# Performance work log

Measured on AMD Instinct MI355X. Metric: run time of the kernel, lower is better.

## Reference

```python
import jax, jax.numpy as jnp
import numpy as np
import math


def _layernorm(x, g, b, eps=1e-5):
    m = x.mean(-1, keepdims=True)
    v = x.var(-1, keepdims=True)
    return (x - m) / jnp.sqrt(v + eps) * g + b


def _ssd(log_decay, frequency, b_r, b_i, chunk):
    # SSD eigenstate evolution: chunk-local complex decay-mask matmuls + sequential inter-chunk state scan
    B, T, K = b_r.shape
    T_pad = -(-T // chunk) * chunk
    if T_pad > T:
        pad = T_pad - T
        b_r = jnp.pad(b_r, ((0, 0), (0, pad), (0, 0)))
        b_i = jnp.pad(b_i, ((0, 0), (0, pad), (0, 0)))
    n_chunks = T_pad // chunk
    mag = jax.nn.sigmoid(log_decay)                      # (K,)
    pos = jnp.arange(chunk, dtype=b_r.dtype)             # (C,)
    mag_pow = mag[None, :] ** pos[:, None]               # (C,K)
    phases = pos[:, None] * frequency[None, :]           # (C,K)
    kernel_r = mag_pow * jnp.cos(phases)
    kernel_i = mag_pow * jnp.sin(phases)
    diffs = pos[None, :] - pos[:, None]                  # (C,C), faithful to torch: pos.unsqueeze(0)-pos.unsqueeze(1)
    mask = (diffs >= 0).astype(b_r.dtype)[:, :, None]
    idx = jnp.clip(diffs, 0, None).astype(jnp.int32)
    L_r = kernel_r[idx] * mask                           # (C,C,K)
    L_i = kernel_i[idx] * mask
    Br = b_r.reshape(B, n_chunks, chunk, K)
    Bi = b_i.reshape(B, n_chunks, chunk, K)
    # intra-chunk complex contraction
    intra_r = jnp.einsum('ijk,bnjk->bnik', L_r, Br) - jnp.einsum('ijk,bnjk->bnik', L_i, Bi)
    intra_i = jnp.einsum('ijk,bnjk->bnik', L_r, Bi) + jnp.einsum('ijk,bnjk->bnik', L_i, Br)
    prop_r = L_r[:, 0, :]                                # (C,K)
    prop_i = L_i[:, 0, :]

    def step(carry, chunk_in):
        sr, si = carry                                   # (B,K)
        ir, ii = chunk_in                                # (B,C,K)
        corr_r = prop_r[None] * sr[:, None] - prop_i[None] * si[:, None]
        corr_i = prop_r[None] * si[:, None] + prop_i[None] * sr[:, None]
        out_r = ir + corr_r
        out_i = ii + corr_i
        return (out_r[:, -1], out_i[:, -1]), (out_r, out_i)

    init = (jnp.zeros((B, K), b_r.dtype), jnp.zeros((B, K), b_r.dtype))
    _, (o_r, o_i) = jax.lax.scan(step, init, (intra_r.transpose(1, 0, 2, 3), intra_i.transpose(1, 0, 2, 3)))
    c_r = o_r.transpose(1, 0, 2, 3).reshape(B, T_pad, K)[:, :T]
    c_i = o_i.transpose(1, 0, 2, 3).reshape(B, T_pad, K)[:, :T]
    return c_r, c_i


def setup_inputs() -> dict:
    B, T, D, K, H, CONV = 4, 4096, 1024, 64, 4, 4
    Kh = K // H
    mlp = 4 * D
    ks = jax.random.split(jax.random.key(0), 12)

    def n(k, shape, s):
        return (jax.random.normal(k, shape) * s).astype(jnp.float32)

    return {
        'x': n(ks[0], (B, T, D), 1.0),
        'in_proj_w': n(ks[1], (2 * K, D), 1.0 / math.sqrt(D)),
        'conv_w': n(ks[2], (2 * K, 1, CONV), 0.5),
        'conv_b': jnp.zeros((2 * K,), jnp.float32),
        'log_decay': jax.random.uniform(ks[3], (K,), minval=-3.0, maxval=-1.5).astype(jnp.float32),
        'frequency': jnp.linspace(0.0, 2 * math.pi * (1 - 1.0 / K), K).astype(jnp.float32),
        'coupling': (jnp.eye(Kh)[None] + 0.01 * jax.random.normal(ks[4], (H, Kh, Kh)) / math.sqrt(Kh)).astype(jnp.float32),
        'out_proj_w': n(ks[5], (D, 2 * K), 1.0 / math.sqrt(2 * K)),
        'gate_w': n(ks[6], (D, D), 1.0 / math.sqrt(D)),
        'gate_b': jnp.full((D,), -2.0, jnp.float32),
        'mlp_w1': n(ks[7], (mlp, D), 1.0 / math.sqrt(D)),
        'mlp_b1': jnp.zeros((mlp,), jnp.float32),
        'mlp_w2': n(ks[8], (D, mlp), 1.0 / math.sqrt(mlp)),
        'mlp_b2': jnp.zeros((D,), jnp.float32),
        'ln1_g': jnp.ones((D,), jnp.float32), 'ln1_b': jnp.zeros((D,), jnp.float32),
        'ln2_g': jnp.ones((D,), jnp.float32), 'ln2_b': jnp.zeros((D,), jnp.float32),
    }


def reference(x, in_proj_w, conv_w, conv_b, log_decay, frequency, coupling,
              out_proj_w, gate_w, gate_b, mlp_w1, mlp_b1, mlp_w2, mlp_b2,
              ln1_g, ln1_b, ln2_g, ln2_b):
    B, T, D = x.shape
    K2 = in_proj_w.shape[0]
    K = K2 // 2
    CHUNK = 64
    H, Kh = coupling.shape[0], coupling.shape[1]
    residual = x
    xn = _layernorm(x, ln1_g, ln1_b)
    beta = xn @ in_proj_w.T                              # (B,T,2K)
    kconv = conv_w.shape[-1]
    # causal depthwise conv1d (torch pads both sides then truncates to T == left-pad kconv-1)
    bc = jax.lax.conv_general_dilated(
        beta.transpose(0, 2, 1), conv_w, (1,), [(kconv - 1, 0)],
        feature_group_count=K2, dimension_numbers=('NCH', 'OIH', 'NCH'))
    beta = jax.nn.silu((bc + conv_b[None, :, None]).transpose(0, 2, 1))
    beta_r, beta_i = beta[..., :K], beta[..., K:]
    c_r, c_i = _ssd(log_decay, frequency, beta_r, beta_i, CHUNK)
    c_r = jnp.einsum('hjk,bthk->bthj', coupling, c_r.reshape(B, T, H, Kh)).reshape(B, T, K)
    c_i = jnp.einsum('hjk,bthk->bthj', coupling, c_i.reshape(B, T, H, Kh)).reshape(B, T, K)
    eig = jnp.concatenate([c_r, c_i], axis=-1)           # (B,T,2K)
    h = eig @ out_proj_w.T
    gate = jax.nn.sigmoid(xn @ gate_w.T + gate_b)
    x1 = residual + gate * h
    xn2 = _layernorm(x1, ln2_g, ln2_b)
    out = x1 + (jax.nn.silu(xn2 @ mlp_w1.T + mlp_b1) @ mlp_w2.T + mlp_b2)
    return out, eig
```

## Files before the change

kernel.cpp:

```cpp
#include <hip/hip_runtime.h>
#include <hip/hip_bf16.h>


#define FIR_LAG 20

typedef __attribute__((ext_vector_type(8))) short    bf16x8;
typedef __attribute__((ext_vector_type(4))) float    f32x4;
typedef __attribute__((ext_vector_type(4))) unsigned short ushort4_t;

__device__ __forceinline__ unsigned short f2bf(float f) {
    union { __hip_bfloat16 b; unsigned short u; } cv;
    cv.b = __float2bfloat16(f);
    return cv.u;
}
__device__ __forceinline__ float bf2f(unsigned short u) {
    return __uint_as_float((unsigned)u << 16);
}

__device__ __forceinline__ void gload_lds16(const unsigned short* g, unsigned short* l) {
    __builtin_amdgcn_global_load_lds(
        (const __attribute__((address_space(1))) unsigned int*)g,
        (__attribute__((address_space(3))) unsigned int*)l, 16, 0, 0);
}

__global__ __launch_bounds__(256) void cvt_bf16_kernel(
    const float* __restrict__ in, unsigned short* __restrict__ out, int n)
{
    int i = (blockIdx.x * 256 + threadIdx.x) * 8;
    if (i >= n) return;
    float4 a = *(const float4*)(in + i);
    float4 b = *(const float4*)(in + i + 4);
    ushort4_t o0 = { f2bf(a.x), f2bf(a.y), f2bf(a.z), f2bf(a.w) };
    ushort4_t o1 = { f2bf(b.x), f2bf(b.y), f2bf(b.z), f2bf(b.w) };
    *(ushort4_t*)(out + i)     = o0;
    *(ushort4_t*)(out + i + 4) = o1;
}

__global__ __launch_bounds__(256) void ln_kernel(
    const float* __restrict__ in, const float* __restrict__ g,
    const float* __restrict__ b, unsigned short* __restrict__ out)
{
    const size_t row = blockIdx.x;
    const int t = threadIdx.x;
    float4 v = ((const float4*)(in + row * 1024))[t];
    float s  = v.x + v.y + v.z + v.w;
    float s2 = v.x*v.x + v.y*v.y + v.z*v.z + v.w*v.w;
    #pragma unroll
    for (int o = 32; o > 0; o >>= 1) {
        s  += __shfl_down(s, o);
        s2 += __shfl_down(s2, o);
    }
    __shared__ float red[8];
    __shared__ float mv[2];
    const int wv = t >> 6;
    if ((t & 63) == 0) { red[wv] = s; red[4 + wv] = s2; }
    __syncthreads();
    if (t == 0) {
        float a  = red[0] + red[1] + red[2] + red[3];
        float a2 = red[4] + red[5] + red[6] + red[7];
        float mean = a * (1.f / 1024.f);
        float var  = a2 * (1.f / 1024.f) - mean * mean;
        mv[0] = mean;
        mv[1] = rsqrtf(var + 1e-5f);
    }
    __syncthreads();
    const float mean = mv[0], rstd = mv[1];
    float4 gg = ((const float4*)g)[t];
    float4 bb = ((const float4*)b)[t];
    ushort4_t o4 = { f2bf((v.x - mean) * rstd * gg.x + bb.x),
                     f2bf((v.y - mean) * rstd * gg.y + bb.y),
                     f2bf((v.z - mean) * rstd * gg.z + bb.z),
                     f2bf((v.w - mean) * rstd * gg.w + bb.w) };
    *(ushort4_t*)(out + row * 1024 + t * 4) = o4;
}

__global__ __launch_bounds__(256) void conv_silu_kernel(
    const float* __restrict__ bp, const float* __restrict__ cw,
    const float* __restrict__ cb, float* __restrict__ beta, int T)
{
    const int idx = blockIdx.x * 256 + threadIdx.x;
    const int c  = idx & 127;
    const int bt = idx >> 7;
    const int t  = bt & (T - 1);
    float acc = cb[c];
    #pragma unroll
    for (int j = 0; j < 4; ++j) {
        int ts = t - 3 + j;
        if (ts >= 0) acc += cw[c * 4 + j] * bp[(size_t)(bt - 3 + j) * 128 + c];
    }
    beta[(size_t)bt * 128 + c] = acc / (1.f + expf(-acc));
}

__global__ __launch_bounds__(256) void fir_coupling_kernel(
    const float* __restrict__ beta, const float* __restrict__ log_decay,
    const float* __restrict__ freq, const float* __restrict__ coup,
    float* __restrict__ eig, unsigned short* __restrict__ eig_bf, int T)
{
    __shared__ float sb[65][128];
    const int blk = blockIdx.x;
    const int nch = T >> 6;
    const int b = blk / nch;
    const int n = blk - b * nch;
    const size_t base = ((size_t)b * T + (size_t)n * 64) * 128;
    const int tid = threadIdx.x;

    #pragma unroll
    for (int it = 0; it < 8; ++it) {
        int f = tid + it * 256;
        int r = f >> 5, c4 = f & 31;
        *(float4*)&sb[1 + r][c4 * 4] =
            *(const float4*)(beta + base + (size_t)r * 128 + c4 * 4);
    }
    if (tid < 32) {
        float4 z = make_float4(0.f, 0.f, 0.f, 0.f);
        *(float4*)&sb[0][tid * 4] =
            (n > 0) ? *(const float4*)(beta + base - 128 + tid * 4) : z;
    }
    __syncthreads();

    const int k  = tid & 63;
    const int tq = tid >> 6;
    const float mag = 1.f / (1.f + expf(-log_decay[k]));
    const float w = freq[k];
    const float rr = mag * cosf(w), ri = mag * sinf(w);
    float cr[16], ci[16];
    #pragma unroll
    for (int m = 0; m < 16; ++m) { cr[m] = 0.f; ci[m] = 0.f; }
    float zr = 1.f, zi = 0.f;
    for (int e = 0; e <= FIR_LAG; ++e) {
        #pragma unroll
        for (int m = 0; m < 16; ++m) {
            int i = tq * 16 + m;
            int src = i + e;
            if (src <= 63) {
                float br = sb[1 + src][k];
                float bi = sb[1 + src][64 + k];
                cr[m] += zr * br - zi * bi;
                ci[m] += zr * bi + zi * br;
            }
        }
        float nzr = zr * rr - zi * ri;
        zi = zr * ri + zi * rr;
        zr = nzr;
    }
    if (tq == 0) {
        cr[0] += sb[0][k];
        ci[0] += sb[0][64 + k];
    }
    __syncthreads();
    #pragma unroll
    for (int m = 0; m < 16; ++m) {
        int i = tq * 16 + m;
        sb[i][k] = cr[m];
        sb[i][64 + k] = ci[m];
    }
    __syncthreads();
    const int h = k >> 4, j = k & 15;
    float cp[16];
    #pragma unroll
    for (int q = 0; q < 16; ++q) cp[q] = coup[(h * 16 + j) * 16 + q];
    #pragma unroll
    for (int m = 0; m < 16; ++m) {
        int i = tq * 16 + m;
        float sr = 0.f, si = 0.f;
        #pragma unroll
        for (int q = 0; q < 16; ++q) {
            sr += cp[q] * sb[i][h * 16 + q];
            si += cp[q] * sb[i][64 + h * 16 + q];
        }
        size_t o = base + (size_t)i * 128;
        eig[o + k]         = sr;
        eig[o + 64 + k]    = si;
        eig_bf[o + k]      = f2bf(sr);
        eig_bf[o + 64 + k] = f2bf(si);
    }
}

__global__ __launch_bounds__(256) void gemm_mfma_f32out(
    const unsigned short* __restrict__ A, const unsigned short* __restrict__ B,
    float* __restrict__ C, int M, int N, int K)
{
    constexpr int BM = 128, BK = 32;
    __shared__ unsigned short As[BM * BK];
    __shared__ unsigned short Bs[BM * BK];
    const int tid  = threadIdx.x;
    const int lane = tid & 63;
    const int wave = tid >> 6;
    const int wm = wave >> 1, wn = wave & 1;
    const int bm = blockIdx.y * BM;
    const int bn = blockIdx.x * BM;

    f32x4 acc[4][4];
    #pragma unroll
    for (int m = 0; m < 4; ++m)
        #pragma unroll
        for (int n = 0; n < 4; ++n) acc[m][n] = (f32x4){0.f, 0.f, 0.f, 0.f};

    const int frow = lane & 15;
    const int fk   = (lane >> 4) * 8;
    const int srow = tid >> 2;
    const int sc   = (tid & 3) * 8;

    for (int k0 = 0; k0 < K; k0 += BK) {
        #pragma unroll
        for (int it = 0; it < 2; ++it) {
            int row = it * 64 + srow;
            int ci  = it * 256 + tid;
            gload_lds16(A + (size_t)(bm + row) * K + k0 + sc, As + ci * 8);
            gload_lds16(B + (size_t)(bn + row) * K + k0 + sc, Bs + ci * 8);
        }
        __syncthreads();
        bf16x8 af[4], bfr[4];
        #pragma unroll
        for (int m = 0; m < 4; ++m)
            af[m] = *(const bf16x8*)(As + (wm * 64 + m * 16 + frow) * BK + fk);
        #pragma unroll
        for (int n = 0; n < 4; ++n)
            bfr[n] = *(const bf16x8*)(Bs + (wn * 64 + n * 16 + frow) * BK + fk);
        #pragma unroll
        for (int m = 0; m < 4; ++m)
            #pragma unroll
            for (int n = 0; n < 4; ++n)
                acc[m][n] = __builtin_amdgcn_mfma_f32_16x16x32_bf16(
                    af[m], bfr[n], acc[m][n], 0, 0, 0);
        __syncthreads();
    }

    const int r0 = (lane >> 4) * 4;
    const int cc = lane & 15;
    #pragma unroll
    for (int m = 0; m < 4; ++m)
        #pragma unroll
        for (int n = 0; n < 4; ++n) {
            const int col = bn + wn * 64 + n * 16 + cc;
            #pragma unroll
            for (int j = 0; j < 4; ++j) {
                const int row = bm + wm * 64 + m * 16 + r0 + j;
                C[(size_t)row * N + col] = acc[m][n][j];
            }
        }
}

template<int EPI, typename OT>
__global__ __launch_bounds__(512) void gemm256(
    const unsigned short* __restrict__ A, const unsigned short* __restrict__ B,
    OT* __restrict__ C, int M, int N, int K,
    const float* __restrict__ bias,
    const float* __restrict__ p1, const unsigned short* __restrict__ p2)
{
    constexpr int BM = 256, BN = 256, BK = 64;
    __shared__ unsigned short As[2][BM * BK];
    __shared__ unsigned short Bs[2][BN * BK];
    const int tid  = threadIdx.x;
    const int lane = tid & 63;
    const int wave = tid >> 6;
    const int wm = wave >> 2;
    const int wn = wave & 3;

    const int nbn = N / BN;
    const int nwg = gridDim.x;
    int orig = blockIdx.x;
    int xcd = orig & 7, ixc = orig >> 3;
    int q = nwg >> 3, r = nwg & 7;
    int wgid = (xcd < r ? xcd * (q + 1) : r * (q + 1) + (xcd - r) * q) + ixc;
    const int bm = (wgid / nbn) * BM;
    const int bn = (wgid % nbn) * BN;

    f32x4 acc[8][4];
    #pragma unroll
    for (int m = 0; m < 8; ++m)
        #pragma unroll
        for (int n = 0; n < 4; ++n) acc[m][n] = (f32x4){0.f, 0.f, 0.f, 0.f};

    const int srow8  = tid >> 3;
    const int schunk = tid & 7;

    const int frow = lane & 15;
    const int l47  = lane & 7;
    const int lk   = lane >> 4;

    const unsigned short* Abase = A + (size_t)bm * K;
    const unsigned short* Bbase = B + (size_t)bn * K;

#define STAGE(G, DS, k0)                                                     \
    {                                                                        \
        _Pragma("unroll")                                                    \
        for (int s = 0; s < 4; ++s) {                                        \
            int row = s * 64 + srow8;                                        \
            int gch = schunk ^ (row & 7);                                    \
            gload_lds16((G) + (size_t)row * K + (k0) + gch * 8,              \
                        (DS) + s * 4096 + tid * 8);                          \
        }                                                                    \
    }

#define LDA(MH)                                                              \
    _Pragma("unroll")                                                        \
    for (int m = 0; m < 4; ++m)                                              \
        _Pragma("unroll")                                                    \
        for (int kk = 0; kk < 2; ++kk)                                       \
            af[m][kk] = *(const bf16x8*)(a_ +                                \
                (wm * 128 + ((MH) * 4 + m) * 16 + frow) * 64 +               \
                ((kk * 4 + lk) ^ l47) * 8);

#define LDB(FR, NH)                                                          \
    _Pragma("unroll")                                                        \
    for (int n = 0; n < 2; ++n)                                              \
        _Pragma("unroll")                                                    \
        for (int kk = 0; kk < 2; ++kk)                                       \
            FR[n][kk] = *(const bf16x8*)(b_ +                                \
                (wn * 64 + ((NH) * 2 + n) * 16 + frow) * 64 +                \
                ((kk * 4 + lk) ^ l47) * 8);

#define PH_MFMA(MH, NH, FR)                                                  \
    asm volatile("s_waitcnt lgkmcnt(0)" ::: "memory");                       \
    __builtin_amdgcn_sched_barrier(0);                                       \
    __builtin_amdgcn_s_setprio(1);                                           \
    _Pragma("unroll")                                                        \
    for (int m = 0; m < 4; ++m)                                              \
        _Pragma("unroll")                                                    \
        for (int n = 0; n < 2; ++n)                                          \
            _Pragma("unroll")                                                \
            for (int kk = 0; kk < 2; ++kk)                                   \
                acc[(MH) * 4 + m][(NH) * 2 + n] =                            \
                    __builtin_amdgcn_mfma_f32_16x16x32_bf16(                 \
                        af[m][kk], FR[n][kk],                                \
                        acc[(MH) * 4 + m][(NH) * 2 + n], 0, 0, 0);           \
    __builtin_amdgcn_s_setprio(0);                                           \
    __builtin_amdgcn_s_barrier();                                            \
    __builtin_amdgcn_sched_barrier(0);

    STAGE(Abase, As[0], 0)
    STAGE(Bbase, Bs[0], 0)

    const int KT = K / BK;
    for (int t = 0; t < KT; ++t) {
        const unsigned short* a_ = As[t & 1];
        const unsigned short* b_ = Bs[t & 1];
        if (t + 1 < KT) {
            STAGE(Abase, As[(t + 1) & 1], (t + 1) * BK)
            STAGE(Bbase, Bs[(t + 1) & 1], (t + 1) * BK)
            asm volatile("s_waitcnt vmcnt(8)" ::: "memory");
        } else {
            asm volatile("s_waitcnt vmcnt(0)" ::: "memory");
        }
        __builtin_amdgcn_s_barrier();
        __builtin_amdgcn_sched_barrier(0);

        bf16x8 af[4][2], bfr0[2][2], bfr1[2][2];
        LDA(0)
        LDB(bfr0, 0)
        PH_MFMA(0, 0, bfr0)
        LDB(bfr1, 1)
        PH_MFMA(0, 1, bfr1)
        LDA(1)
        PH_MFMA(1, 1, bfr1)
        PH_MFMA(1, 0, bfr0)
    }
#undef STAGE
#undef LDA
#undef LDB
#undef PH_MFMA

    const int r0 = (lane >> 4) * 4;
    const int cc = lane & 15;
    #pragma unroll
    for (int m = 0; m < 8; ++m) {
        #pragma unroll
        for (int n = 0; n < 4; ++n) {
            const int col = bn + wn * 64 + n * 16 + cc;
            #pragma unroll
            for (int j = 0; j < 4; ++j) {
                const int row = bm + wm * 128 + m * 16 + r0 + j;
                const size_t idx = (size_t)row * N + col;
                const float v = acc[m][n][j];
                if constexpr (EPI == 0) {
                    C[idx] = v;
                } else if constexpr (EPI == 1) {
                    float pre = v + bias[col];
                    float gt = 1.f / (1.f + expf(-pre));
                    C[idx] = p1[idx] + gt * bf2f(p2[idx]);
                } else if constexpr (EPI == 2) {
                    float pre = v + bias[col];
                    C[idx] = (OT)__float2bfloat16(pre / (1.f + expf(-pre)));
                } else if constexpr (EPI == 3) {
                    C[idx] = p1[idx] + v + bias[col];
                } else {
                    C[idx] = (OT)__float2bfloat16(v);
                }
            }
        }
    }
}

extern "C" void kernel_launch(void* const* d_in, const int* in_sizes, int n_in,
                              void* d_out, int out_size, void* d_ws, size_t ws_size,
                              hipStream_t stream)
{
    const float* x        = (const float*)d_in[0];
    const float* in_proj  = (const float*)d_in[1];
    const float* conv_w   = (const float*)d_in[2];
    const float* conv_b   = (const float*)d_in[3];
    const float* log_dec  = (const float*)d_in[4];
    const float* freq     = (const float*)d_in[5];
    const float* coup     = (const float*)d_in[6];
    const float* out_proj = (const float*)d_in[7];
    const float* gate_w   = (const float*)d_in[8];
    const float* gate_b   = (const float*)d_in[9];
    const float* mlp_w1   = (const float*)d_in[10];
    const float* mlp_b1   = (const float*)d_in[11];
    const float* mlp_w2   = (const float*)d_in[12];
    const float* mlp_b2   = (const float*)d_in[13];
    const float* ln1_g    = (const float*)d_in[14];
    const float* ln1_b    = (const float*)d_in[15];
    const float* ln2_g    = (const float*)d_in[16];
    const float* ln2_b    = (const float*)d_in[17];

    const int B = 4, T = 4096, D = 1024;
    const int M = B * T;

    float* out = (float*)d_out;
    float* eig = out + (size_t)M * D;
    float* bpre = eig;

    char* w = (char*)d_ws;
    unsigned short* xn_bf = (unsigned short*)w; w += (size_t)M * 1024 * 2;
    float* x1             = (float*)w;          w += (size_t)M * 1024 * 4;
    float* beta           = (float*)w;          w += (size_t)M * 128 * 4;
    unsigned short* mid   = (unsigned short*)w; w += (size_t)M * 4096 * 2;
    unsigned short* eig_bf= (unsigned short*)w; w += (size_t)M * 128 * 2;
    unsigned short* wb_inproj = (unsigned short*)w; w += (size_t)128 * 1024 * 2;
    unsigned short* wb_outproj= (unsigned short*)w; w += (size_t)1024 * 128 * 2;
    unsigned short* wb_gate   = (unsigned short*)w; w += (size_t)1024 * 1024 * 2;
    unsigned short* wb_mlp1   = (unsigned short*)w; w += (size_t)4096 * 1024 * 2;
    unsigned short* wb_mlp2   = (unsigned short*)w; w += (size_t)1024 * 4096 * 2;
    unsigned short* h_bf = mid;

    cvt_bf16_kernel<<<(128 * 1024) / 2048, 256, 0, stream>>>(in_proj, wb_inproj, 128 * 1024);
    cvt_bf16_kernel<<<(1024 * 128) / 2048, 256, 0, stream>>>(out_proj, wb_outproj, 1024 * 128);
    cvt_bf16_kernel<<<(1024 * 1024) / 2048, 256, 0, stream>>>(gate_w, wb_gate, 1024 * 1024);
    cvt_bf16_kernel<<<(4096 * 1024) / 2048, 256, 0, stream>>>(mlp_w1, wb_mlp1, 4096 * 1024);
    cvt_bf16_kernel<<<(1024 * 4096) / 2048, 256, 0, stream>>>(mlp_w2, wb_mlp2, 1024 * 4096);

    ln_kernel<<<M, 256, 0, stream>>>(x, ln1_g, ln1_b, xn_bf);
    gemm_mfma_f32out<<<dim3(1, M / 128), 256, 0, stream>>>(
        xn_bf, wb_inproj, bpre, M, 128, 1024);
    conv_silu_kernel<<<(M * 128) / 256, 256, 0, stream>>>(bpre, conv_w, conv_b, beta, T);
    fir_coupling_kernel<<<B * (T / 64), 256, 0, stream>>>(
        beta, log_dec, freq, coup, eig, eig_bf, T);
    gemm256<4, __hip_bfloat16><<<(M / 256) * (1024 / 256), 512, 0, stream>>>(
        eig_bf, wb_outproj, (__hip_bfloat16*)h_bf, M, 1024, 128,
        nullptr, nullptr, nullptr);
    gemm256<1, float><<<(M / 256) * (1024 / 256), 512, 0, stream>>>(
        xn_bf, wb_gate, x1, M, 1024, 1024, gate_b, x, h_bf);
    ln_kernel<<<M, 256, 0, stream>>>(x1, ln2_g, ln2_b, xn_bf);
    gemm256<2, __hip_bfloat16><<<(M / 256) * (4096 / 256), 512, 0, stream>>>(
        xn_bf, wb_mlp1, (__hip_bfloat16*)mid, M, 4096, 1024, mlp_b1, nullptr, nullptr);
    gemm256<3, float><<<(M / 256) * (1024 / 256), 512, 0, stream>>>(
        mid, wb_mlp2, out, M, 1024, 4096, mlp_b2, x1, nullptr);
}
```

Measured before the change: 598.1 us.

## Restructure gemm256 into a 4-deep K=32 LDS ring with split staging

Replaces the double-buffered BK=64 LDS tiles in the 256x256 GEMM with a four-slot ring of BK=32 half-tiles, prefetching three slices ahead. A and B loads for the next slice are issued between the two MFMA phases, using a new XOR swizzle on 4-chunk rows. The goal is to hide global-load latency better and overlap loads with MFMA work at the same LDS footprint. The cost is more barriers per unit of K and finer vmcnt bookkeeping.

Measured after the change: 563.5 us. -5.8%, faster.

```diff
diff --git a/kernel.cpp b/kernel.cpp
--- a/kernel.cpp
+++ b/kernel.cpp
@@ -248,9 +248,9 @@
     const float* __restrict__ bias,
     const float* __restrict__ p1, const unsigned short* __restrict__ p2)
 {
-    constexpr int BM = 256, BN = 256, BK = 64;
-    __shared__ unsigned short As[2][BM * BK];
-    __shared__ unsigned short Bs[2][BN * BK];
+    constexpr int BM = 256, BN = 256;
+    __shared__ unsigned short Asw[4 * 256 * 32];
+    __shared__ unsigned short Bsw[4 * 256 * 32];
     const int tid  = threadIdx.x;
     const int lane = tid & 63;
     const int wave = tid >> 6;
@@ -272,94 +272,97 @@
         #pragma unroll
         for (int n = 0; n < 4; ++n) acc[m][n] = (f32x4){0.f, 0.f, 0.f, 0.f};
 
-    const int srow8  = tid >> 3;
-    const int schunk = tid & 7;
-
-    const int frow = lane & 15;
-    const int l47  = lane & 7;
-    const int lk   = lane >> 4;
+    const int frow   = lane & 15;
+    const int lk     = lane >> 4;
+    const int achunk = lk ^ (frow & 3);
 
     const unsigned short* Abase = A + (size_t)bm * K;
     const unsigned short* Bbase = B + (size_t)bn * K;
 
-#define STAGE(G, DS, k0)                                                     \
+#define STAGE_H(G, DS, KH)                                                   \
     {                                                                        \
         _Pragma("unroll")                                                    \
-        for (int s = 0; s < 4; ++s) {                                        \
-            int row = s * 64 + srow8;                                        \
-            int gch = schunk ^ (row & 7);                                    \
-            gload_lds16((G) + (size_t)row * K + (k0) + gch * 8,              \
-                        (DS) + s * 4096 + tid * 8);                          \
+        for (int s = 0; s < 2; ++s) {                                        \
+            int cid = s * 512 + tid;                                         \
+            int row = cid >> 2, c = cid & 3;                                 \
+            int gch = c ^ (row & 3);                                         \
+            gload_lds16((G) + (size_t)row * K + (KH) * 32 + gch * 8,         \
+                        (DS) + ((KH) & 3) * 8192 + cid * 8);                 \
         }                                                                    \
     }
 
-#define LDA(MH)                                                              \
+#define LDA(MH, KH)                                                          \
     _Pragma("unroll")                                                        \
-    for (int m = 0; m < 4; ++m)                                              \
-        _Pragma("unroll")                                                    \
-        for (int kk = 0; kk < 2; ++kk)                                       \
-            af[m][kk] = *(const bf16x8*)(a_ +                                \
-                (wm * 128 + ((MH) * 4 + m) * 16 + frow) * 64 +               \
-                ((kk * 4 + lk) ^ l47) * 8);
-
-#define LDB(FR, NH)                                                          \
+    for (int m = 0; m < 4; ++m) {                                            \
+        int row = wm * 128 + (MH) * 64 + m * 16 + frow;                      \
+        af[m] = *(const bf16x8*)(Asw + ((KH) & 3) * 8192 + row * 32 +        \
+                                 achunk * 8);                                \
+    }
+
+#define LDB(KH)                                                              \
     _Pragma("unroll")                                                        \
-    for (int n = 0; n < 2; ++n)                                              \
-        _Pragma("unroll")                                                    \
-        for (int kk = 0; kk < 2; ++kk)                                       \
-            FR[n][kk] = *(const bf16x8*)(b_ +                                \
-                (wn * 64 + ((NH) * 2 + n) * 16 + frow) * 64 +                \
-                ((kk * 4 + lk) ^ l47) * 8);
-
-#define PH_MFMA(MH, NH, FR)                                                  \
+    for (int n = 0; n < 4; ++n) {                                            \
+        int row = wn * 64 + n * 16 + frow;                                   \
+        bfv[n] = *(const bf16x8*)(Bsw + ((KH) & 3) * 8192 + row * 32 +       \
+                                  achunk * 8);                               \
+    }
+
+#define BARRIER                                                              \
+    asm volatile("s_barrier" ::: "memory");                                  \
+    __builtin_amdgcn_sched_barrier(0);
+
+#define MFMA_PH(MH)                                                          \
     asm volatile("s_waitcnt lgkmcnt(0)" ::: "memory");                       \
     __builtin_amdgcn_sched_barrier(0);                                       \
     __builtin_amdgcn_s_setprio(1);                                           \
     _Pragma("unroll")                                                        \
     for (int m = 0; m < 4; ++m)                                              \
         _Pragma("unroll")                                                    \
-        for (int n = 0; n < 2; ++n)                                          \
-            _Pragma("unroll")                                                \
-            for (int kk = 0; kk < 2; ++kk)                                   \
-                acc[(MH) * 4 + m][(NH) * 2 + n] =                            \
-                    __builtin_amdgcn_mfma_f32_16x16x32_bf16(                 \
-                        af[m][kk], FR[n][kk],                                \
-                        acc[(MH) * 4 + m][(NH) * 2 + n], 0, 0, 0);           \
-    __builtin_amdgcn_s_setprio(0);                                           \
-    __builtin_amdgcn_s_barrier();                                            \
-    __builtin_amdgcn_sched_barrier(0);
-
-    STAGE(Abase, As[0], 0)
-    STAGE(Bbase, Bs[0], 0)
-
-    const int KT = K / BK;
-    for (int t = 0; t < KT; ++t) {
-        const unsigned short* a_ = As[t & 1];
-        const unsigned short* b_ = Bs[t & 1];
-        if (t + 1 < KT) {
-            STAGE(Abase, As[(t + 1) & 1], (t + 1) * BK)
-            STAGE(Bbase, Bs[(t + 1) & 1], (t + 1) * BK)
-            asm volatile("s_waitcnt vmcnt(8)" ::: "memory");
-        } else {
-            asm volatile("s_waitcnt vmcnt(0)" ::: "memory");
-        }
-        __builtin_amdgcn_s_barrier();
-        __builtin_amdgcn_sched_barrier(0);
-
-        bf16x8 af[4][2], bfr0[2][2], bfr1[2][2];
-        LDA(0)
-        LDB(bfr0, 0)
-        PH_MFMA(0, 0, bfr0)
-        LDB(bfr1, 1)
-        PH_MFMA(0, 1, bfr1)
-        LDA(1)
-        PH_MFMA(1, 1, bfr1)
-        PH_MFMA(1, 0, bfr0)
-    }
-#undef STAGE
+        for (int n = 0; n < 4; ++n)                                          \
+            acc[(MH) * 4 + m][n] = __builtin_amdgcn_mfma_f32_16x16x32_bf16(  \
+                af[m], bfv[n], acc[(MH) * 4 + m][n], 0, 0, 0);               \
+    __builtin_amdgcn_s_setprio(0);
+
+    const int NKH = K >> 5;
+
+    STAGE_H(Abase, Asw, 0)
+    STAGE_H(Bbase, Bsw, 0)
+    STAGE_H(Abase, Asw, 1)
+    STAGE_H(Bbase, Bsw, 1)
+    STAGE_H(Abase, Asw, 2)
+    STAGE_H(Bbase, Bsw, 2)
+    asm volatile("s_waitcnt vmcnt(8)" ::: "memory");
+    BARRIER
+
+    for (int kh = 0; kh < NKH; ++kh) {
+        bf16x8 af[4], bfv[4];
+        LDA(0, kh)
+        LDB(kh)
+        if (kh + 3 < NKH) { STAGE_H(Abase, Asw, kh + 3) }
+        BARRIER
+        MFMA_PH(0)
+        BARRIER
+        LDA(1, kh)
+        if (kh + 3 < NKH) { STAGE_H(Bbase, Bsw, kh + 3) }
+        {
+            int rem = NKH - 1 - kh;
+            if (rem >= 3) {
+                asm volatile("s_waitcnt vmcnt(8)" ::: "memory");
+            } else if (rem == 2) {
+                asm volatile("s_waitcnt vmcnt(4)" ::: "memory");
+            } else if (rem == 1) {
+                asm volatile("s_waitcnt vmcnt(0)" ::: "memory");
+            }
+        }
+        BARRIER
+        MFMA_PH(1)
+        BARRIER
+    }
+#undef STAGE_H
 #undef LDA
 #undef LDB
-#undef PH_MFMA
+#undef BARRIER
+#undef MFMA_PH
 
     const int r0 = (lane >> 4) * 4;
     const int cc = lane & 15;
```
